# Kernel optimization log

Measured on AMD Instinct MI355X. Metric: run time of the kernel, lower is better.

## Reference

```python
import jax, jax.numpy as jnp
import numpy as np

N = 50000
E = 1600000
IN_C = 32
OUT_C = 32
OUT_SIZE = 1


def setup_inputs() -> dict:
    key = jax.random.key(0)
    ks = jax.random.split(key, 16)
    x = jax.random.normal(ks[0], (N, IN_C), dtype=jnp.float32)
    edge_index = jax.random.randint(ks[1], (2, E), 0, N, dtype=jnp.int64)

    def glorot(k, shape):
        lim = float(np.sqrt(6.0 / (shape[0] + shape[1])))
        return jax.random.uniform(k, shape, jnp.float32, -lim, lim)

    params = {
        # GCNConv weights for gates z, r, h: [in, out] and bias [out]
        'Wz_c': glorot(ks[2], (IN_C, OUT_C)), 'bz_c': jnp.zeros((OUT_C,), jnp.float32),
        'Wr_c': glorot(ks[3], (IN_C, OUT_C)), 'br_c': jnp.zeros((OUT_C,), jnp.float32),
        'Wh_c': glorot(ks[4], (IN_C, OUT_C)), 'bh_c': jnp.zeros((OUT_C,), jnp.float32),
        # GRU linear layers: [2*out, out] and bias [out]
        'Wz_l': glorot(ks[5], (2 * OUT_C, OUT_C)), 'bz_l': jnp.zeros((OUT_C,), jnp.float32),
        'Wr_l': glorot(ks[6], (2 * OUT_C, OUT_C)), 'br_l': jnp.zeros((OUT_C,), jnp.float32),
        'Wh_l': glorot(ks[7], (2 * OUT_C, OUT_C)), 'bh_l': jnp.zeros((OUT_C,), jnp.float32),
        # final readout Linear(out_channels, output_size)
        'W_lin': glorot(ks[8], (OUT_C, OUT_SIZE)), 'b_lin': jnp.zeros((OUT_SIZE,), jnp.float32),
    }
    return {'x': x, 'edge_index': edge_index, **params}


def _gcn_conv(x, W, b, src, dst, n_nodes):
    """GCNConv with add_self_loops=False, symmetric normalization."""
    h = x @ W  # [N, out]
    ones = jnp.ones((src.shape[0],), h.dtype)
    deg = jax.ops.segment_sum(ones, dst, num_segments=n_nodes)  # in-degree at targets
    dinv = jnp.where(deg > 0, jax.lax.rsqrt(jnp.maximum(deg, 1e-12)), 0.0)
    norm = dinv[src] * dinv[dst]  # [E]
    msg = h[src] * norm[:, None]  # gather + scale
    agg = jax.ops.segment_sum(msg, dst, num_segments=n_nodes)  # scatter-add
    return agg + b


def reference(x, edge_index, Wz_c, bz_c, Wr_c, br_c, Wh_c, bh_c,
              Wz_l, bz_l, Wr_l, br_l, Wh_l, bh_l, W_lin, b_lin):
    src, dst = edge_index[0], edge_index[1]
    n = x.shape[0]
    H = jnp.zeros((n, OUT_C), x.dtype)  # H=None -> zeros

    Z = jax.nn.sigmoid(jnp.concatenate([_gcn_conv(x, Wz_c, bz_c, src, dst, n), H], axis=1) @ Wz_l + bz_l)
    R = jax.nn.sigmoid(jnp.concatenate([_gcn_conv(x, Wr_c, br_c, src, dst, n), H], axis=1) @ Wr_l + br_l)
    H_tilde = jnp.tanh(jnp.concatenate([_gcn_conv(x, Wh_c, bh_c, src, dst, n), H * R], axis=1) @ Wh_l + bh_l)
    H = Z * H + (1.0 - Z) * H_tilde

    h = jax.nn.relu(H)
    return h @ W_lin + b_lin  # [N, output_size]
```

## Files before the change

### kernel.cpp

```cpp
#include <hip/hip_runtime.h>
#include <hip/hip_fp16.h>
#include <math.h>

#define NN 50000
#define NE 1600000
#define ELLW 80
#define SHN 6250
#define XH_WORDS 800000

#define NBIN 400
#define BINW 125
#define NSUB 8
#define SUBCAP 680
#define MAGIC125 34359739u

#define OFF_ELL 0
#define NEED_A ((4000000ull + 800000 + 800000 + 50000 + 2112) * 4)
#define NEED_B ((4000000ull + 800000 + 50000 + 2112) * 4)

struct h2x2 { __half2 a, b; };

__global__ __launch_bounds__(1024) void init_kernel(
        const float* __restrict__ Wz_c, const float* __restrict__ bz_c,
        const float* __restrict__ Wh_c, const float* __restrict__ bh_c,
        const float* __restrict__ Wz_l, const float* __restrict__ bz_l,
        const float* __restrict__ Wh_l, const float* __restrict__ bh_l,
        float* __restrict__ Mz, float* __restrict__ Mh,
        float* __restrict__ cz, float* __restrict__ ch,
        unsigned int* __restrict__ bcur,
        const float* __restrict__ x, __half2* __restrict__ xh) {
    int t = threadIdx.x;
    if (blockIdx.x == 0) {
        int i = t >> 5, j = t & 31;
        float az = 0.0f, ah = 0.0f;
        for (int k = 0; k < 32; ++k) {
            az += Wz_c[i * 32 + k] * Wz_l[k * 32 + j];
            ah += Wh_c[i * 32 + k] * Wh_l[k * 32 + j];
        }
        Mz[i * 32 + j] = az;
        Mh[i * 32 + j] = ah;
        if (i == 0) {
            float sz = bz_l[j], sh = bh_l[j];
            for (int k = 0; k < 32; ++k) {
                sz += bz_c[k] * Wz_l[k * 32 + j];
                sh += bh_c[k] * Wh_l[k * 32 + j];
            }
            cz[j] = sz;
            ch[j] = sh;
        }
        return;
    }
    if (blockIdx.x == 1) {
        for (int i = t; i < NBIN * NSUB; i += 1024) bcur[i] = 0u;
    }
    if (xh) {
        int idx = (blockIdx.x - 1) * 1024 + t;
        int stride = (gridDim.x - 1) * 1024;
        const float2* x2 = (const float2*)x;
        for (int i = idx; i < XH_WORDS; i += stride) {
            float2 v = x2[i];
            xh[i] = __floats2half2_rn(v.x, v.y);
        }
    }
}

__global__ __launch_bounds__(512) void bucket_kernel(const int* __restrict__ ei,
                                                     unsigned int* __restrict__ bcur,
                                                     unsigned int* __restrict__ bkt) {
    __shared__ unsigned int lcnt[NBIN];
    __shared__ unsigned int lstart[NBIN];
    __shared__ unsigned int loff[NBIN];
    __shared__ unsigned int gbase[NBIN];
    __shared__ unsigned int stage[2048];
    int t = threadIdx.x;
    for (int i = t; i < NBIN; i += 512) lcnt[i] = 0u;
    __syncthreads();
    int i4 = blockIdx.x * 512 + t;
    bool valid = (i4 < NE / 4);
    int4 s4 = make_int4(0, 0, 0, 0), d4 = make_int4(0, 0, 0, 0);
    if (valid) {
        s4 = ((const int4*)ei)[i4];
        d4 = ((const int4*)(ei + NE))[i4];
#define CNT_E(dd)                                                           \
        if ((unsigned)(dd) < NN)                                            \
            atomicAdd(&lcnt[__umulhi((unsigned)(dd), MAGIC125)], 1u);
        CNT_E(d4.x) CNT_E(d4.y) CNT_E(d4.z) CNT_E(d4.w)
#undef CNT_E
    }
    __syncthreads();
    if (t < NBIN) loff[t] = lcnt[t];
    __syncthreads();
    for (int off = 1; off < NBIN; off <<= 1) {
        unsigned v = 0;
        if (t < NBIN && t >= off) v = loff[t - off];
        __syncthreads();
        if (t < NBIN) loff[t] += v;
        __syncthreads();
    }
    int g = blockIdx.x & (NSUB - 1);
    if (t < NBIN) {
        lstart[t] = loff[t] - lcnt[t];
        gbase[t] = lcnt[t] ? atomicAdd(&bcur[t * NSUB + g], lcnt[t]) : 0u;
    }
    __syncthreads();
    if (t < NBIN) loff[t] = lstart[t];
    __syncthreads();
    if (valid) {
#define SC_E(dd, ss)                                                        \
        if ((unsigned)(dd) < NN && (unsigned)(ss) < NN) {                   \
            unsigned bn = __umulhi((unsigned)(dd), MAGIC125);               \
            unsigned p = atomicAdd(&loff[bn], 1u);                          \
            stage[p] = ((unsigned)(dd) << 16) | (unsigned)(ss);             \
        }
        SC_E(d4.x, s4.x) SC_E(d4.y, s4.y) SC_E(d4.z, s4.z) SC_E(d4.w, s4.w)
#undef SC_E
    }
    __syncthreads();
    unsigned tot = loff[NBIN - 1];
    for (unsigned i = t; i < tot; i += 512) {
        unsigned v = stage[i];
        unsigned bn = __umulhi(v >> 16, MAGIC125);
        unsigned gg = gbase[bn] + (i - lstart[bn]);
        if (gg < SUBCAP) bkt[(bn * NSUB + g) * SUBCAP + gg] = v;
    }
}

__global__ __launch_bounds__(256) void build_ell_kernel(const unsigned int* __restrict__ bkt,
                                                        const unsigned int* __restrict__ bcur,
                                                        unsigned int* __restrict__ cnt,
                                                        float* __restrict__ dinv,
                                                        unsigned short* __restrict__ ell) {
    __shared__ unsigned int lcnt[BINW];
    __shared__ alignas(16) unsigned short stage[BINW * ELLW];
    int t = threadIdx.x;
    int b = blockIdx.x;
    int bin = (b & 7) * 50 + (b >> 3);
    int nbase = bin * BINW;
    for (int i = t; i < BINW; i += 256) lcnt[i] = 0u;
    __syncthreads();
    for (int g = 0; g < NSUB; ++g) {
        unsigned tot = bcur[bin * NSUB + g];
        if (tot > SUBCAP) tot = SUBCAP;
        const unsigned int* bp = bkt + (bin * NSUB + g) * SUBCAP;
        for (unsigned i = t; i < tot; i += 256) {
            unsigned v = bp[i];
            unsigned ld = (v >> 16) - (unsigned)nbase;
            unsigned p = atomicAdd(&lcnt[ld], 1u);
            if (p < ELLW) stage[ld * ELLW + p] = (unsigned short)(v & 0xffffu);
        }
    }
    __syncthreads();
    const uint2* st2 = (const uint2*)stage;
    uint2* ell2 = (uint2*)(ell + (size_t)nbase * ELLW);
    for (int i = t; i < BINW * ELLW / 4; i += 256) ell2[i] = st2[i];
    for (int i = t; i < BINW; i += 256) {
        unsigned d = lcnt[i];
        cnt[nbase + i] = d;
        dinv[nbase + i] = d ? rsqrtf((float)d) : 0.0f;
    }
}

template <int USE_H>
__global__ __launch_bounds__(256) void gather_node_kernel(const unsigned short* __restrict__ ell,
                                                          const unsigned int* __restrict__ cnt,
                                                          const float* __restrict__ dinv,
                                                          const float* __restrict__ x,
                                                          const h2x2* __restrict__ xh,
                                                          const float* __restrict__ Mz,
                                                          const float* __restrict__ Mh,
                                                          const float* __restrict__ cz,
                                                          const float* __restrict__ ch,
                                                          const float* __restrict__ Wlin,
                                                          const float* __restrict__ blin,
                                                          float* __restrict__ out) {
    __shared__ float sMz[1024], sMh[1024], scz[32], sch[32], sw[32];
    __shared__ float xs[8][32];
    int t = threadIdx.x;
    for (int i = t; i < 1024; i += 256) { sMz[i] = Mz[i]; sMh[i] = Mh[i]; }
    if (t < 32) { scz[t] = cz[t]; sch[t] = ch[t]; sw[t] = Wlin[t]; }
    __syncthreads();

    int l    = t & 63;
    int slot = t >> 5;
    int q    = l & 31;
    int hb   = l & 32;
    int shard = blockIdx.x & 7;
    int grp   = blockIdx.x >> 3;
    int ns = grp * 8 + slot;
    if (ns >= SHN) return;
    int n = shard * SHN + ns;

    int base = n * ELLW;
    int len0 = (int)cnt[n];
    float dn = len0 ? rsqrtf((float)len0) : 0.0f;
    int len = len0 > ELLW ? ELLW : len0;
    int lenW = max(len, __shfl_xor(len, 32));

    const float4* x4 = (const float4*)x;
    int es = q >> 3;
    int k  = q & 7;
    float4 acc = make_float4(0.f, 0.f, 0.f, 0.f);

    for (int c0 = 0; c0 < lenW; c0 += 32) {
        int m = len - c0; if (m > 32) m = 32;
        int mw = lenW - c0; if (mw > 32) mw = 32;
        int s = 0; float wgt = 0.0f;
        if (q < m) { s = (int)ell[base + c0 + q]; wgt = dinv[s]; }
#define SW(j0) { int sl = hb + (j0) + es; int sj = __shfl(s, sl); float wj = __shfl(wgt, sl); \
                 if (USE_H) {                                                              \
                     h2x2 hv = xh[sj * 8 + k];                                             \
                     float2 f0 = __half22float2(hv.a), f1 = __half22float2(hv.b);          \
                     acc.x += f0.x * wj; acc.y += f0.y * wj;                               \
                     acc.z += f1.x * wj; acc.w += f1.y * wj;                               \
                 } else {                                                                  \
                     float4 v = x4[sj * 8 + k];                                            \
                     acc.x += v.x * wj; acc.y += v.y * wj;                                 \
                     acc.z += v.z * wj; acc.w += v.w * wj;                                 \
                 } }
        SW(0) SW(4)
        if (mw > 8)  { SW(8)  SW(12) }
        if (mw > 16) { SW(16) SW(20) }
        if (mw > 24) { SW(24) SW(28) }
#undef SW
    }
    #pragma unroll
    for (int mm = 8; mm <= 16; mm <<= 1) {
        acc.x += __shfl_xor(acc.x, mm);
        acc.y += __shfl_xor(acc.y, mm);
        acc.z += __shfl_xor(acc.z, mm);
        acc.w += __shfl_xor(acc.w, mm);
    }
    if (es == 0) {
        float4* xs4 = (float4*)&xs[slot][0];
        xs4[k] = make_float4(acc.x * dn, acc.y * dn, acc.z * dn, acc.w * dn);
    }

    int j = q;
    float az = scz[j];
    float ah = sch[j];
    #pragma unroll
    for (int i = 0; i < 32; ++i) {
        float v = xs[slot][i];
        az += v * sMz[i * 32 + j];
        ah += v * sMh[i * 32 + j];
    }
    float z  = 1.0f / (1.0f + __expf(-az));
    float ht = tanhf(ah);
    float hv = (1.0f - z) * ht;
    hv = hv > 0.0f ? hv : 0.0f;
    float val = hv * sw[j];
    val += __shfl_xor(val, 1);
    val += __shfl_xor(val, 2);
    val += __shfl_xor(val, 4);
    val += __shfl_xor(val, 8);
    val += __shfl_xor(val, 16);
    if (q == 0) out[n] = val + blin[0];
}

extern "C" void kernel_launch(void* const* d_in, const int* in_sizes, int n_in,
                              void* d_out, int out_size, void* d_ws, size_t ws_size,
                              hipStream_t stream) {
    const float* x    = (const float*)d_in[0];
    const int*   ei   = (const int*)d_in[1];
    const float* Wz_c = (const float*)d_in[2];
    const float* bz_c = (const float*)d_in[3];
    const float* Wh_c = (const float*)d_in[6];
    const float* bh_c = (const float*)d_in[7];
    const float* Wz_l = (const float*)d_in[8];
    const float* bz_l = (const float*)d_in[9];
    const float* Wh_l = (const float*)d_in[12];
    const float* bh_l = (const float*)d_in[13];
    const float* Wlin = (const float*)d_in[14];
    const float* blin = (const float*)d_in[15];
    float* out = (float*)d_out;
    float* ws = (float*)d_ws;

    int use_h = (ws_size >= NEED_A) ? 1 : 0;

    unsigned short* ell16 = (unsigned short*)(ws + OFF_ELL);
    unsigned int*   cnt   = (unsigned int*)(ws + 2000000);
    __half2*        xh    = use_h ? (__half2*)(ws + 2050000) : nullptr;
    float*          dinv  = ws + 2050000 + (use_h ? XH_WORDS : 0);
    float*          Mz    = dinv + NN;
    float*          Mh    = Mz + 1024;
    float*          cz    = Mh + 1024;
    float*          ch    = cz + 32;
    unsigned int*   bkt   = (unsigned int*)(ch + 32);
    unsigned int*   bcur  = bkt + (size_t)NBIN * NSUB * SUBCAP;

    const int bucket_grid = (NE / 4 + 511) / 512;
    const int build_grid  = NBIN;
    const int node_grid   = 8 * ((SHN + 7) / 8);
    const int init_grid   = 1 + 256;

    init_kernel<<<init_grid, 1024, 0, stream>>>(Wz_c, bz_c, Wh_c, bh_c,
                                                Wz_l, bz_l, Wh_l, bh_l,
                                                Mz, Mh, cz, ch, bcur, x, xh);
    bucket_kernel<<<bucket_grid, 512, 0, stream>>>(ei, bcur, bkt);
    build_ell_kernel<<<build_grid, 256, 0, stream>>>(bkt, bcur, cnt, dinv, ell16);
    if (use_h) {
        gather_node_kernel<1><<<node_grid, 256, 0, stream>>>(
            ell16, cnt, dinv, x, (const h2x2*)xh, Mz, Mh, cz, ch, Wlin, blin, out);
    } else {
        gather_node_kernel<0><<<node_grid, 256, 0, stream>>>(
            ell16, cnt, dinv, x, (const h2x2*)nullptr, Mz, Mh, cz, ch, Wlin, blin, out);
    }
}
```

Measured before the change: 159.5 us.

## Replace global-atomic sub-bucket scatter with per-block sorted chunks and offset headers

The bucket kernel now writes each block's locally bin-sorted 2048 edges contiguously, plus a per-block header of bin offsets, instead of reserving space with global atomics into capped sub-buckets. This drops the bcur counters and their zeroing. The init work (weight folding and the x-to-half conversion) moves into extra blocks of the bucket kernel, removing one launch. In exchange, build_ell must scan the headers of all 782 blocks for each bin, with each thread serially walking a short range of edges.

After: 152.2 us. -4.6%, faster.

```diff
diff --git a/kernel.cpp b/kernel.cpp
--- a/kernel.cpp
+++ b/kernel.cpp
@@ -10,81 +10,76 @@
 
 #define NBIN 400
 #define BINW 125
-#define NSUB 8
-#define SUBCAP 680
+#define NBLK 782
+#define HDRW 404
 #define MAGIC125 34359739u
 
-#define OFF_ELL 0
 #define NEED_A ((4000000ull + 800000 + 800000 + 50000 + 2112) * 4)
 #define NEED_B ((4000000ull + 800000 + 50000 + 2112) * 4)
 
 struct h2x2 { __half2 a, b; };
 
-__global__ __launch_bounds__(1024) void init_kernel(
+__global__ __launch_bounds__(512) void bucket_kernel(
+        const int* __restrict__ ei,
+        unsigned int* __restrict__ bkt, unsigned int* __restrict__ hdr,
         const float* __restrict__ Wz_c, const float* __restrict__ bz_c,
         const float* __restrict__ Wh_c, const float* __restrict__ bh_c,
         const float* __restrict__ Wz_l, const float* __restrict__ bz_l,
         const float* __restrict__ Wh_l, const float* __restrict__ bh_l,
         float* __restrict__ Mz, float* __restrict__ Mh,
         float* __restrict__ cz, float* __restrict__ ch,
-        unsigned int* __restrict__ bcur,
         const float* __restrict__ x, __half2* __restrict__ xh) {
     int t = threadIdx.x;
-    if (blockIdx.x == 0) {
-        int i = t >> 5, j = t & 31;
-        float az = 0.0f, ah = 0.0f;
-        for (int k = 0; k < 32; ++k) {
-            az += Wz_c[i * 32 + k] * Wz_l[k * 32 + j];
-            ah += Wh_c[i * 32 + k] * Wh_l[k * 32 + j];
-        }
-        Mz[i * 32 + j] = az;
-        Mh[i * 32 + j] = ah;
-        if (i == 0) {
-            float sz = bz_l[j], sh = bh_l[j];
-            for (int k = 0; k < 32; ++k) {
-                sz += bz_c[k] * Wz_l[k * 32 + j];
-                sh += bh_c[k] * Wh_l[k * 32 + j];
+    int b = blockIdx.x;
+    if (b >= NBLK) {
+        if (b == NBLK) {
+            for (int p = t; p < 1024; p += 512) {
+                int i = p >> 5, j = p & 31;
+                float az = 0.0f, ah = 0.0f;
+                for (int k = 0; k < 32; ++k) {
+                    az += Wz_c[i * 32 + k] * Wz_l[k * 32 + j];
+                    ah += Wh_c[i * 32 + k] * Wh_l[k * 32 + j];
+                }
+                Mz[p] = az;
+                Mh[p] = ah;
             }
-            cz[j] = sz;
-            ch[j] = sh;
+            if (t < 32) {
+                int j = t;
+                float sz = bz_l[j], sh = bh_l[j];
+                for (int k = 0; k < 32; ++k) {
+                    sz += bz_c[k] * Wz_l[k * 32 + j];
+                    sh += bh_c[k] * Wh_l[k * 32 + j];
+                }
+                cz[j] = sz;
+                ch[j] = sh;
+            }
+        } else if (xh) {
+            int idx = (b - NBLK - 1) * 512 + t;
+            int stride = (gridDim.x - NBLK - 1) * 512;
+            const float2* x2 = (const float2*)x;
+            for (int i = idx; i < XH_WORDS; i += stride) {
+                float2 v = x2[i];
+                xh[i] = __floats2half2_rn(v.x, v.y);
+            }
         }
         return;
     }
-    if (blockIdx.x == 1) {
-        for (int i = t; i < NBIN * NSUB; i += 1024) bcur[i] = 0u;
-    }
-    if (xh) {
-        int idx = (blockIdx.x - 1) * 1024 + t;
-        int stride = (gridDim.x - 1) * 1024;
-        const float2* x2 = (const float2*)x;
-        for (int i = idx; i < XH_WORDS; i += stride) {
-            float2 v = x2[i];
-            xh[i] = __floats2half2_rn(v.x, v.y);
-        }
-    }
-}
-
-__global__ __launch_bounds__(512) void bucket_kernel(const int* __restrict__ ei,
-                                                     unsigned int* __restrict__ bcur,
-                                                     unsigned int* __restrict__ bkt) {
     __shared__ unsigned int lcnt[NBIN];
     __shared__ unsigned int lstart[NBIN];
     __shared__ unsigned int loff[NBIN];
-    __shared__ unsigned int gbase[NBIN];
-    __shared__ unsigned int stage[2048];
-    int t = threadIdx.x;
+    __shared__ alignas(16) unsigned int stage[2048];
     for (int i = t; i < NBIN; i += 512) lcnt[i] = 0u;
     __syncthreads();
-    int i4 = blockIdx.x * 512 + t;
+    int i4 = b * 512 + t;
     bool valid = (i4 < NE / 4);
     int4 s4 = make_int4(0, 0, 0, 0), d4 = make_int4(0, 0, 0, 0);
     if (valid) {
         s4 = ((const int4*)ei)[i4];
         d4 = ((const int4*)(ei + NE))[i4];
-#define CNT_E(dd)                                                           \
-        if ((unsigned)(dd) < NN)                                            \
+#define CNT_E(dd, ss)                                                       \
+        if ((unsigned)(dd) < NN && (unsigned)(ss) < NN)                     \
             atomicAdd(&lcnt[__umulhi((unsigned)(dd), MAGIC125)], 1u);
-        CNT_E(d4.x) CNT_E(d4.y) CNT_E(d4.z) CNT_E(d4.w)
+        CNT_E(d4.x, s4.x) CNT_E(d4.y, s4.y) CNT_E(d4.z, s4.z) CNT_E(d4.w, s4.w)
 #undef CNT_E
     }
     __syncthreads();
@@ -97,11 +92,11 @@
         if (t < NBIN) loff[t] += v;
         __syncthreads();
     }
-    int g = blockIdx.x & (NSUB - 1);
     if (t < NBIN) {
         lstart[t] = loff[t] - lcnt[t];
-        gbase[t] = lcnt[t] ? atomicAdd(&bcur[t * NSUB + g], lcnt[t]) : 0u;
-    }
+        hdr[b * HDRW + t] = loff[t] - lcnt[t];
+    }
+    if (t == 0) hdr[b * HDRW + NBIN] = loff[NBIN - 1];
     __syncthreads();
     if (t < NBIN) loff[t] = lstart[t];
     __syncthreads();
@@ -116,33 +111,27 @@
 #undef SC_E
     }
     __syncthreads();
-    unsigned tot = loff[NBIN - 1];
-    for (unsigned i = t; i < tot; i += 512) {
-        unsigned v = stage[i];
-        unsigned bn = __umulhi(v >> 16, MAGIC125);
-        unsigned gg = gbase[bn] + (i - lstart[bn]);
-        if (gg < SUBCAP) bkt[(bn * NSUB + g) * SUBCAP + gg] = v;
-    }
+    ((uint4*)bkt)[b * 512 + t] = ((const uint4*)stage)[t];
 }
 
 __global__ __launch_bounds__(256) void build_ell_kernel(const unsigned int* __restrict__ bkt,
-                                                        const unsigned int* __restrict__ bcur,
+                                                        const unsigned int* __restrict__ hdr,
                                                         unsigned int* __restrict__ cnt,
                                                         float* __restrict__ dinv,
                                                         unsigned short* __restrict__ ell) {
     __shared__ unsigned int lcnt[BINW];
     __shared__ alignas(16) unsigned short stage[BINW * ELLW];
     int t = threadIdx.x;
-    int b = blockIdx.x;
-    int bin = (b & 7) * 50 + (b >> 3);
+    int blk = blockIdx.x;
+    int bin = (blk & 7) * 50 + (blk >> 3);
     int nbase = bin * BINW;
     for (int i = t; i < BINW; i += 256) lcnt[i] = 0u;
     __syncthreads();
-    for (int g = 0; g < NSUB; ++g) {
-        unsigned tot = bcur[bin * NSUB + g];
-        if (tot > SUBCAP) tot = SUBCAP;
-        const unsigned int* bp = bkt + (bin * NSUB + g) * SUBCAP;
-        for (unsigned i = t; i < tot; i += 256) {
+    for (int b = t; b < NBLK; b += 256) {
+        unsigned o0 = hdr[b * HDRW + bin];
+        unsigned o1 = hdr[b * HDRW + bin + 1];
+        const unsigned int* bp = bkt + b * 2048;
+        for (unsigned i = o0; i < o1; ++i) {
             unsigned v = bp[i];
             unsigned ld = (v >> 16) - (unsigned)nbase;
             unsigned p = atomicAdd(&lcnt[ld], 1u);
@@ -277,7 +266,7 @@
 
     int use_h = (ws_size >= NEED_A) ? 1 : 0;
 
-    unsigned short* ell16 = (unsigned short*)(ws + OFF_ELL);
+    unsigned short* ell16 = (unsigned short*)(ws);
     unsigned int*   cnt   = (unsigned int*)(ws + 2000000);
     __half2*        xh    = use_h ? (__half2*)(ws + 2050000) : nullptr;
     float*          dinv  = ws + 2050000 + (use_h ? XH_WORDS : 0);
@@ -286,18 +275,17 @@
     float*          cz    = Mh + 1024;
     float*          ch    = cz + 32;
     unsigned int*   bkt   = (unsigned int*)(ch + 32);
-    unsigned int*   bcur  = bkt + (size_t)NBIN * NSUB * SUBCAP;
-
-    const int bucket_grid = (NE / 4 + 511) / 512;
-    const int build_grid  = NBIN;
-    const int node_grid   = 8 * ((SHN + 7) / 8);
-    const int init_grid   = 1 + 256;
-
-    init_kernel<<<init_grid, 1024, 0, stream>>>(Wz_c, bz_c, Wh_c, bh_c,
-                                                Wz_l, bz_l, Wh_l, bh_l,
-                                                Mz, Mh, cz, ch, bcur, x, xh);
-    bucket_kernel<<<bucket_grid, 512, 0, stream>>>(ei, bcur, bkt);
-    build_ell_kernel<<<build_grid, 256, 0, stream>>>(bkt, bcur, cnt, dinv, ell16);
+    unsigned int*   hdr   = bkt + (size_t)NBLK * 2048;
+
+    const int k1_grid   = NBLK + 1 + (use_h ? 225 : 0);
+    const int build_grid = NBIN;
+    const int node_grid  = 8 * ((SHN + 7) / 8);
+
+    bucket_kernel<<<k1_grid, 512, 0, stream>>>(ei, bkt, hdr,
+                                               Wz_c, bz_c, Wh_c, bh_c,
+                                               Wz_l, bz_l, Wh_l, bh_l,
+                                               Mz, Mh, cz, ch, x, xh);
+    build_ell_kernel<<<build_grid, 256, 0, stream>>>(bkt, hdr, cnt, dinv, ell16);
     if (use_h) {
         gather_node_kernel<1><<<node_grid, 256, 0, stream>>>(
             ell16, cnt, dinv, x, (const h2x2*)xh, Mz, Mh, cz, ch, Wlin, blin, out);
```
